# Performance work log

Hardware: AMD Instinct MI355X
Metric: run time of the kernel (lower is better)

The kernel has to match this reference:

```python
import jax, jax.numpy as jnp
import numpy as np

N_FFT = 512
HOP = 128
REF_MIC = 0
B, C, T = 8, 8, 64000


def hann(n):
    # periodic Hann, like torch.hann_window
    return 0.5 - 0.5 * jnp.cos(2.0 * jnp.pi * jnp.arange(n) / n)


def stft(x, n_fft, hop, window):
    # torch.stft with center=True, reflect padding, onesided
    pad = n_fft // 2
    pads = [(0, 0)] * (x.ndim - 1) + [(pad, pad)]
    xp = jnp.pad(x, pads, mode="reflect")
    n_frames = 1 + (xp.shape[-1] - n_fft) // hop
    idx = jnp.arange(n_frames)[:, None] * hop + jnp.arange(n_fft)[None, :]
    frames = xp[..., idx] * window                  # (..., N, n_fft)
    X = jnp.fft.rfft(frames, axis=-1)               # (..., N, F)
    return jnp.swapaxes(X, -1, -2)                  # (..., F, N)


def istft(X, n_fft, hop, window):
    # torch.istft: windowed overlap-add with squared-window normalization
    pad = n_fft // 2
    Xt = jnp.swapaxes(X, -1, -2)                    # (..., N, F)
    frames = jnp.fft.irfft(Xt, n=n_fft, axis=-1) * window  # (..., N, n_fft)
    n_frames = frames.shape[-2]
    out_len = n_fft + hop * (n_frames - 1)
    idx = jnp.arange(n_frames)[:, None] * hop + jnp.arange(n_fft)[None, :]
    y = jnp.zeros(frames.shape[:-2] + (out_len,), frames.dtype).at[..., idx].add(frames)
    wsum = jnp.zeros((out_len,), frames.dtype).at[idx].add(
        jnp.broadcast_to(window ** 2, (n_frames, n_fft)))
    y = y / jnp.maximum(wsum, 1e-10)
    return y[..., pad:out_len - pad]                # undo center padding


def mwf_forward(x, w1, b1, w2, b2):
    window = hann(N_FFT).astype(x.dtype)
    X = stft(x, N_FFT, HOP, window)                 # (B, C, F, N) complex
    X = X[..., 1:, :]                               # drop DC bin -> F' = n_fft//2
    b, c, fp, n = X.shape
    # --- mask model: 2-layer MLP on |X_ref| over frequency, per frame ---
    Xref = X[..., REF_MIC, :, :]                    # (B, F', N)
    feat = jnp.abs(Xref).swapaxes(-1, -2)           # (B, N, F')
    h = jax.nn.relu(feat @ w1 + b1)                 # (B, N, H)
    m = jax.nn.sigmoid(h @ w2 + b2)                 # (B, N, 2*F')
    masks = m.reshape(b, n, 2, fp).transpose(0, 2, 3, 1)[:, None]  # (B,1,2,F',N)
    mask_t = masks[..., 0, :, :]                    # (B, 1, F', N)
    mask_n = masks[..., 1, :, :]
    # --- masked spatial covariance matrices ---
    R_tgt = jnp.einsum("bsfn,bcfn,bdfn->bsfcd", mask_t, X, X.conj())
    R_noise = jnp.einsum("bsfn,bcfn,bdfn->bsfcd", mask_n, X, X.conj())
    # --- MWF beamforming weights: (R_t + R_n)^{-1} R_t e_ref ---
    rhs = R_tgt[..., REF_MIC]                       # (B, 1, F', C)
    bf = jnp.linalg.solve(R_tgt + R_noise, rhs[..., None])[..., 0]
    Xe = jnp.einsum("bcfn,bsfc->bsfn", X, bf.conj())  # (B, 1, F', N)
    # pad DC bin back with zeros
    Xe = jnp.concatenate([jnp.zeros(Xe.shape[:-2] + (1, n), Xe.dtype), Xe], axis=-2)
    y = istft(Xe, N_FFT, HOP, window)               # (B, 1, T')
    t = x.shape[-1]
    if y.shape[-1] < t:
        y = jnp.concatenate(
            [y, jnp.zeros(y.shape[:-1] + (t - y.shape[-1],), y.dtype)], axis=-1)
    else:
        y = y[..., :t]
    return y


def setup_inputs() -> dict:
    key = jax.random.key(0)
    k1, k2, k3 = jax.random.split(key, 3)
    fp, hid = N_FFT // 2, 512
    x = jax.random.normal(k1, (B, C, T), dtype=jnp.float32)
    w1 = jax.random.normal(k2, (fp, hid), dtype=jnp.float32) * (1.0 / np.sqrt(fp))
    b1 = jnp.zeros((hid,), dtype=jnp.float32)
    w2 = jax.random.normal(k3, (hid, 2 * fp), dtype=jnp.float32) * (1.0 / np.sqrt(hid))
    b2 = jnp.zeros((2 * fp,), dtype=jnp.float32)
    return {"x": x, "w1": w1, "b1": b1, "w2": w2, "b2": b2}


def reference(x, w1, b1, w2, b2):
    return mwf_forward(x, w1, b1, w2, b2)
```

## Files before the change

### kernel.cpp

```cpp
#include <hip/hip_runtime.h>
#include <hip/hip_bf16.h>
#include <math.h>

#define NFFT 512
#define HOP  128
#define PADW 256
#define TLEN 64000
#define NF   501
#define NFP  504
#define FP   256
#define CH   8
#define BATCH 8
#define HID  512
#define MROWS (BATCH * NF)
#define FPB  8
#define NGRP 63
#define CNCK 8
#define CCK  63
#define NSTG 4

#define S2C 0.70710678118654752f

typedef short bf16x8 __attribute__((ext_vector_type(8)));
typedef float f32x4 __attribute__((ext_vector_type(4)));

__device__ __forceinline__ unsigned short f2bf(float v) {
    __hip_bfloat16 hb = __float2bfloat16(v);
    return *reinterpret_cast<unsigned short*>(&hb);
}

__device__ __forceinline__ float2 cadd(float2 a, float2 b) { return make_float2(a.x + b.x, a.y + b.y); }
__device__ __forceinline__ float2 csub(float2 a, float2 b) { return make_float2(a.x - b.x, a.y - b.y); }
__device__ __forceinline__ float2 cmul(float2 a, float2 b) { return make_float2(a.x * b.x - a.y * b.y, a.x * b.y + a.y * b.x); }
__device__ __forceinline__ float2 mulnegi(float2 a) { return make_float2(a.y, -a.x); }

__device__ __forceinline__ void dft8(const float2 u[8], float2 v[8]) {
    float2 a0 = cadd(u[0], u[4]), a1 = cadd(u[1], u[5]), a2 = cadd(u[2], u[6]), a3 = cadd(u[3], u[7]);
    float2 b0 = csub(u[0], u[4]), b1 = csub(u[1], u[5]), b2 = csub(u[2], u[6]), b3 = csub(u[3], u[7]);
    float2 c0 = cadd(a0, a2), c1 = csub(a0, a2), c2 = cadd(a1, a3), c3 = csub(a1, a3);
    v[0] = cadd(c0, c2); v[4] = csub(c0, c2);
    float2 nic3 = mulnegi(c3);
    v[2] = cadd(c1, nic3); v[6] = csub(c1, nic3);
    float2 d1 = make_float2(S2C * (b1.x + b1.y), S2C * (b1.y - b1.x));
    float2 d2 = mulnegi(b2);
    float2 d3 = make_float2(S2C * (b3.y - b3.x), -S2C * (b3.x + b3.y));
    float2 e0 = cadd(b0, d2), e1 = csub(b0, d2), e2 = cadd(d1, d3), e3 = csub(d1, d3);
    v[1] = cadd(e0, e2); v[5] = csub(e0, e2);
    float2 nie3 = mulnegi(e3);
    v[3] = cadd(e1, nie3); v[7] = csub(e1, nie3);
}

__device__ __forceinline__ int refl(int j) {
    j = (j < 0) ? -j : j;
    j = (j >= TLEN) ? 2 * (TLEN - 1) - j : j;
    return j;
}

__global__ void k_tables(float* tw) {
    int j = threadIdx.x + blockIdx.x * blockDim.x;
    if (j < 512) {
        float ang = (float)(2.0 * M_PI * (double)j / 512.0);
        tw[j] = 0.5f - 0.5f * cosf(ang);
    }
}

__global__ __launch_bounds__(256) void k_wt(const float* __restrict__ w,
                                            unsigned short* __restrict__ wt, int K) {
    __shared__ float tile[32][33];
    int nt = blockIdx.x & 15;
    int kt = blockIdx.x >> 4;
    int tx = threadIdx.x & 31, ty = threadIdx.x >> 5;
    #pragma unroll
    for (int r = 0; r < 4; ++r)
        tile[ty + 8 * r][tx] = w[(size_t)(kt * 32 + ty + 8 * r) * HID + nt * 32 + tx];
    __syncthreads();
    #pragma unroll
    for (int r = 0; r < 4; ++r)
        wt[(size_t)(nt * 32 + ty + 8 * r) * K + kt * 32 + tx] = f2bf(tile[tx][ty + 8 * r]);
}

#define A_S 580
#define B_S 544
__global__ __launch_bounds__(256, 4) void k_stft(const float* __restrict__ x,
                                                 const float* __restrict__ tw,
                                                 float2* __restrict__ X,
                                                 unsigned short* __restrict__ featbf) {
    __shared__ float2 Abuf[4 * A_S];
    __shared__ float2 Bbuf[4 * B_S];
    __shared__ float2 Twd[512];
    int blk = blockIdx.x;
    int g = blk % NGRP;
    int bc = blk / NGRP;
    int c = bc % CH, b = bc / CH;
    int m0 = g * FPB;
    int tid = threadIdx.x;
    const float* xp = x + (size_t)(b * CH + c) * TLEN;

    #pragma unroll
    for (int r = 0; r < 2; ++r) {
        int e = tid + 256 * r;
        float se, ce;
        sincosf((float)e * (float)(2.0 * M_PI / 512.0), &se, &ce);
        Twd[e] = make_float2(ce, -se);
    }

    #pragma unroll
    for (int r = 0; r < 8; ++r) {
        int flat = r * 256 + tid;
        int sig = flat >> 9, t = flat & 511;
        int posa = (m0 + 2 * sig) * HOP + t - PADW;
        float xa = xp[refl(posa)];
        float xb = xp[refl(posa + HOP)];
        float w = tw[t];
        Abuf[sig * A_S + t] = make_float2(xa * w, xb * w);
    }
    __syncthreads();

    int sig = tid >> 6, dft = tid & 63;
    float2 u[8], v[8];

    {
        const float2* Az = &Abuf[sig * A_S];
        float2* Bu = &Bbuf[sig * B_S];
        #pragma unroll
        for (int a = 0; a < 8; ++a) u[a] = Az[64 * a + dft];
        dft8(u, v);
        #pragma unroll
        for (int k0 = 0; k0 < 8; ++k0) Bu[k0 * 68 + dft] = v[k0];
    }
    __syncthreads();

    {
        int k0 = dft >> 3, cd = dft & 7;
        const float2* Bu = &Bbuf[sig * B_S];
        float2* Au = &Abuf[sig * A_S];
        #pragma unroll
        for (int bb = 0; bb < 8; ++bb) u[bb] = Bu[k0 * 68 + 8 * bb + cd];
        #pragma unroll
        for (int bb = 1; bb < 8; ++bb) u[bb] = cmul(u[bb], Twd[(8 * bb * k0) & 511]);
        dft8(u, v);
        #pragma unroll
        for (int k1 = 0; k1 < 8; ++k1) Au[(8 * k0 + k1) * 9 + cd] = v[k1];
    }
    __syncthreads();

    {
        int k0 = dft >> 3, k1 = dft & 7;
        int kk = k0 + 8 * k1;
        const float2* Au = &Abuf[sig * A_S];
        float2* Bz = &Bbuf[sig * B_S];
        #pragma unroll
        for (int cd = 0; cd < 8; ++cd) u[cd] = Au[dft * 9 + cd];
        #pragma unroll
        for (int cd = 1; cd < 8; ++cd) u[cd] = cmul(u[cd], Twd[(cd * kk) & 511]);
        dft8(u, v);
        #pragma unroll
        for (int k2 = 0; k2 < 8; ++k2) Bz[kk + 64 * k2] = v[k2];
    }
    __syncthreads();

    {
        int kp = tid;
        int k = kp + 1;
        #pragma unroll
        for (int s = 0; s < 4; ++s) {
            float2 z1 = Bbuf[s * B_S + k];
            float2 z2 = Bbuf[s * B_S + (512 - k)];
            float Ar = 0.5f * (z1.x + z2.x);
            float Ai = 0.5f * (z1.y - z2.y);
            float Br = 0.5f * (z1.y + z2.y);
            float Bi = 0.5f * (z2.x - z1.x);
            int ma = m0 + 2 * s, mb_ = ma + 1;
            if (ma < NF) {
                X[((size_t)(b * NF + ma) * CH + c) * FP + kp] = make_float2(Ar, Ai);
                if (c == 0) featbf[((size_t)b * NF + ma) * FP + kp] = f2bf(sqrtf(Ar * Ar + Ai * Ai));
            }
            if (mb_ < NF) {
                X[((size_t)(b * NF + mb_) * CH + c) * FP + kp] = make_float2(Br, Bi);
                if (c == 0) featbf[((size_t)b * NF + mb_) * FP + kp] = f2bf(sqrtf(Br * Br + Bi * Bi));
            }
        }
    }
}

template<int K, int ACT>
__global__ __launch_bounds__(256) void k_mfma_mlp(const unsigned short* __restrict__ Abf,
                                                  const unsigned short* __restrict__ Wt,
                                                  const float* __restrict__ bias,
                                                  float* __restrict__ outf,
                                                  unsigned short* __restrict__ outbf,
                                                  int M) {
    __shared__ unsigned short Al[64][40];
    __shared__ unsigned short Bl[128][40];
    int bid = blockIdx.x;
    int nt = bid & 3, mt = bid >> 2;
    int m0 = mt * 64, n0 = nt * 128;
    int tid = threadIdx.x;
    int wid = tid >> 6, lane = tid & 63;
    int wm = wid >> 1, wn = wid & 1;
    int lr = lane & 15, lk = (lane >> 4) * 8;

    f32x4 acc[2][4] = {};

    int arow = tid >> 2, ak = (tid & 3) * 8;
    for (int k0 = 0; k0 < K; k0 += 32) {
        int garow = m0 + arow; if (garow > M - 1) garow = M - 1;
        float4 av = *(const float4*)&Abf[(size_t)garow * K + k0 + ak];
        int s0 = tid, s1 = tid + 256;
        float4 bv0 = *(const float4*)&Wt[(size_t)(n0 + (s0 >> 2)) * K + k0 + (s0 & 3) * 8];
        float4 bv1 = *(const float4*)&Wt[(size_t)(n0 + (s1 >> 2)) * K + k0 + (s1 & 3) * 8];
        if (k0 > 0) __syncthreads();
        *(float4*)&Al[arow][ak] = av;
        *(float4*)&Bl[s0 >> 2][(s0 & 3) * 8] = bv0;
        *(float4*)&Bl[s1 >> 2][(s1 & 3) * 8] = bv1;
        __syncthreads();
        bf16x8 af[2], bfr[4];
        af[0] = *(const bf16x8*)&Al[wm * 32 + lr][lk];
        af[1] = *(const bf16x8*)&Al[wm * 32 + 16 + lr][lk];
        #pragma unroll
        for (int nf = 0; nf < 4; ++nf)
            bfr[nf] = *(const bf16x8*)&Bl[wn * 64 + nf * 16 + lr][lk];
        #pragma unroll
        for (int mf = 0; mf < 2; ++mf)
            #pragma unroll
            for (int nf = 0; nf < 4; ++nf)
                acc[mf][nf] = __builtin_amdgcn_mfma_f32_16x16x32_bf16(af[mf], bfr[nf], acc[mf][nf], 0, 0, 0);
    }

    int rbase = (lane >> 4) * 4;
    #pragma unroll
    for (int mf = 0; mf < 2; ++mf) {
        #pragma unroll
        for (int nf = 0; nf < 4; ++nf) {
            int n = n0 + wn * 64 + nf * 16 + lr;
            float bj = bias[n];
            #pragma unroll
            for (int r = 0; r < 4; ++r) {
                int m = m0 + wm * 32 + mf * 16 + rbase + r;
                if (m < M) {
                    float vv = acc[mf][nf][r] + bj;
                    if (ACT == 0) {
                        outbf[(size_t)m * HID + n] = f2bf(fmaxf(vv, 0.f));
                    } else {
                        outf[(size_t)m * HID + n] = 1.f / (1.f + expf(-vv));
                    }
                }
            }
        }
    }
}

__global__ __launch_bounds__(512) void k_cov(const float2* __restrict__ X,
                                             const float* __restrict__ mo,
                                             float2* __restrict__ part) {
    int blk = blockIdx.x;
    int nc = blk & 7;
    int ftile = (blk >> 3) & 3;
    int b = blk >> 5;
    int tid = threadIdx.x;
    int c = tid >> 6;
    int ft = tid & 63;
    int f = ftile * 64 + ft;
    int n0 = nc * CCK;
    int n1 = n0 + CCK; if (n1 > NF) n1 = NF;

    __shared__ float2 vbuf[2][NSTG][CH][64];

    float ar[8], ai[8];
    #pragma unroll
    for (int d = 0; d < 8; ++d) { ar[d] = 0.f; ai[d] = 0.f; }
    float rr = 0.f, ri = 0.f;

    const float2* Xb = X + (size_t)b * NF * CH * FP;
    const float* mb = mo + (size_t)b * NF * HID;

    #pragma unroll
    for (int r = 0; r < NSTG; ++r) {
        int n = n0 + r;
        if (n < n1) vbuf[0][r][c][ft] = Xb[(size_t)(n * CH + c) * FP + f];
    }
    __syncthreads();
    int cur = 0;
    for (int nb = n0; nb < n1; nb += NSTG) {
        int nbn = nb + NSTG;
        float2 nx[NSTG];
        #pragma unroll
        for (int r = 0; r < NSTG; ++r) {
            int n = nbn + r;
            if (n < n1) nx[r] = Xb[(size_t)(n * CH + c) * FP + f];
        }
        float mts[NSTG], mns[NSTG];
        #pragma unroll
        for (int r = 0; r < NSTG; ++r) {
            int n = nb + r;
            if (n < n1) {
                mts[r] = mb[(size_t)n * HID + f];
                mns[r] = mb[(size_t)n * HID + FP + f];
            }
        }
        #pragma unroll
        for (int r = 0; r < NSTG; ++r) {
            int n = nb + r;
            if (n < n1) {
                float mt = mts[r], mn = mns[r];
                float w = mt + mn;
                float2 xc = vbuf[cur][r][c][ft];
                #pragma unroll
                for (int d = 0; d < 8; ++d) {
                    float2 xd = vbuf[cur][r][d][ft];
                    float pr = xc.x * xd.x + xc.y * xd.y;
                    float pi = xc.y * xd.x - xc.x * xd.y;
                    ar[d] += w * pr; ai[d] += w * pi;
                    if (d == 0) { rr += mt * pr; ri += mt * pi; }
                }
            }
        }
        if (nbn < n1) {
            #pragma unroll
            for (int r = 0; r < NSTG; ++r) {
                int n = nbn + r;
                if (n < n1) vbuf[cur ^ 1][r][c][ft] = nx[r];
            }
        }
        __syncthreads();
        cur ^= 1;
    }
    float2* pp = part + (((size_t)nc * BATCH + b) * FP + f) * 72;
    #pragma unroll
    for (int d = 0; d < 8; ++d)
        pp[c * 8 + d] = make_float2(ar[d], ai[d]);
    pp[64 + c] = make_float2(rr, ri);
}

__global__ __launch_bounds__(512) void k_cov_solve2(const float2* __restrict__ part,
                                                    float2* __restrict__ wc) {
    int blk = blockIdx.x;
    int fg = blk & 31;
    int b = blk >> 5;
    int tid = threadIdx.x;
    int c = tid >> 6, d = (tid >> 3) & 7, fl = tid & 7;
    int f = fg * 8 + fl;
    float ar = 0.f, ai = 0.f, rr = 0.f, ri = 0.f;
    const float2* pb = part + ((size_t)b * FP + f) * 72;
    #pragma unroll
    for (int nc = 0; nc < CNCK; ++nc) {
        const float2* p = pb + (size_t)nc * BATCH * FP * 72;
        float2 v = p[c * 8 + d];
        ar += v.x; ai += v.y;
        if (d == 0) { float2 u = p[64 + c]; rr += u.x; ri += u.y; }
    }
    __shared__ float2 Am[8][73];
    __shared__ float2 rh[8][8];
    __shared__ float2 sl[8][9];
    Am[fl][c * 9 + d] = make_float2(ar, ai);
    if (d == 0) rh[fl][c] = make_float2(rr, ri);
    __syncthreads();
    if (tid < 8) {
        int ln = tid;
        float2* A = Am[ln];
        float2* r = rh[ln];
        float2* sol = sl[ln];
        for (int kk = 0; kk < 8; ++kk) {
            float2 pp = A[kk * 9 + kk];
            float ip = 1.f / (pp.x * pp.x + pp.y * pp.y);
            float invr = pp.x * ip, invi = -pp.y * ip;
            for (int i = kk + 1; i < 8; ++i) {
                float2 aik = A[i * 9 + kk];
                float fr2 = aik.x * invr - aik.y * invi;
                float fi2 = aik.x * invi + aik.y * invr;
                for (int jj = kk; jj < 8; ++jj) {
                    float2 ak = A[kk * 9 + jj];
                    A[i * 9 + jj].x -= fr2 * ak.x - fi2 * ak.y;
                    A[i * 9 + jj].y -= fr2 * ak.y + fi2 * ak.x;
                }
                r[i].x -= fr2 * r[kk].x - fi2 * r[kk].y;
                r[i].y -= fr2 * r[kk].y + fi2 * r[kk].x;
            }
        }
        for (int kk = 7; kk >= 0; --kk) {
            float sr = r[kk].x, si = r[kk].y;
            for (int jj = kk + 1; jj < 8; ++jj) {
                float2 ak = A[kk * 9 + jj];
                float2 xj = sol[jj];
                sr -= ak.x * xj.x - ak.y * xj.y;
                si -= ak.x * xj.y + ak.y * xj.x;
            }
            float2 pp = A[kk * 9 + kk];
            float ip = 1.f / (pp.x * pp.x + pp.y * pp.y);
            sol[kk].x = (sr * pp.x + si * pp.y) * ip;
            sol[kk].y = (si * pp.x - sr * pp.y) * ip;
        }
        for (int cc = 0; cc < 8; ++cc)
            wc[((size_t)b * CH + cc) * FP + fg * 8 + ln] = make_float2(sol[cc].x, -sol[cc].y);
    }
}

__global__ __launch_bounds__(512) void k_istft_bf(const float2* __restrict__ X,
                                                  const float2* __restrict__ wc,
                                                  float* __restrict__ yfr) {
    __shared__ float2 Zp[4 * 512];
    __shared__ float2 Gl[16 * 32 * 5];
    int blk = blockIdx.x;
    int g = blk % NGRP, b = blk / NGRP;
    int m0 = g * FPB;
    int tid = threadIdx.x;

    if (tid < 4) Zp[tid * 512] = make_float2(0.f, 0.f);
    const float2* Xb0 = X + (size_t)b * NF * CH * FP;
    const float2* wcb = wc + (size_t)b * CH * FP;
    #pragma unroll
    for (int half = 0; half < 2; ++half) {
        int i = half * 512 + tid;
        int sig = i >> 8, kp = i & 255;
        int ma = m0 + 2 * sig, mb_ = ma + 1;
        float2 Xa = make_float2(0.f, 0.f), Xb = make_float2(0.f, 0.f);
        if (ma < NF) {
            #pragma unroll
            for (int c = 0; c < 8; ++c) {
                float2 xv = Xb0[(size_t)(ma * CH + c) * FP + kp];
                float2 wv = wcb[c * FP + kp];
                Xa.x += xv.x * wv.x - xv.y * wv.y;
                Xa.y += xv.x * wv.y + xv.y * wv.x;
            }
        }
        if (mb_ < NF) {
            #pragma unroll
            for (int c = 0; c < 8; ++c) {
                float2 xv = Xb0[(size_t)(mb_ * CH + c) * FP + kp];
                float2 wv = wcb[c * FP + kp];
                Xb.x += xv.x * wv.x - xv.y * wv.y;
                Xb.y += xv.x * wv.y + xv.y * wv.x;
            }
        }
        int k = kp + 1;
        if (k == 256) {
            Zp[sig * 512 + 256] = make_float2(Xa.x, Xb.x);
        } else {
            Zp[sig * 512 + k]       = make_float2(Xa.x - Xb.y, Xa.y + Xb.x);
            Zp[sig * 512 + 512 - k] = make_float2(Xa.x + Xb.y, Xb.x - Xa.y);
        }
    }
    __syncthreads();

    {
        int k1 = tid >> 5, tau = tid & 31;
        float sa, ca;
        sincosf((float)tau * (float)(2.0 * M_PI / 32.0), &sa, &ca);
        float stepc = ca, steps = sa;
        float gr[4], gi[4];
        #pragma unroll
        for (int s = 0; s < 4; ++s) { gr[s] = 0.f; gi[s] = 0.f; }
        float cr = 1.f, ci = 0.f;
        #pragma unroll 4
        for (int k2 = 0; k2 < 32; ++k2) {
            int k = k1 + 16 * k2;
            #pragma unroll
            for (int s = 0; s < 4; ++s) {
                float2 z = Zp[s * 512 + k];
                gr[s] += z.x * cr - z.y * ci;
                gi[s] += z.x * ci + z.y * cr;
            }
            float ncr = cr * stepc - ci * steps;
            ci = cr * steps + ci * stepc;
            cr = ncr;
        }
        #pragma unroll
        for (int s = 0; s < 4; ++s)
            Gl[(k1 * 32 + tau) * 5 + s] = make_float2(gr[s], gi[s]);
    }
    __syncthreads();

    int t = tid;
    int tau = t & 31;
    float sa2, ca2;
    sincosf((float)t * (float)(2.0 * M_PI / 512.0), &sa2, &ca2);
    float stepc = ca2, steps = sa2;
    float accr[4], acci[4];
    #pragma unroll
    for (int s = 0; s < 4; ++s) { accr[s] = 0.f; acci[s] = 0.f; }
    float cr = 1.f, ci = 0.f;
    #pragma unroll 4
    for (int k1 = 0; k1 < 16; ++k1) {
        #pragma unroll
        for (int s = 0; s < 4; ++s) {
            float2 gv = Gl[(k1 * 32 + tau) * 5 + s];
            accr[s] += gv.x * cr - gv.y * ci;
            acci[s] += gv.x * ci + gv.y * cr;
        }
        float ncr = cr * stepc - ci * steps;
        ci = cr * steps + ci * stepc;
        cr = ncr;
    }
    float wv = (0.5f - 0.5f * ca2) * (1.f / 512.f);
    #pragma unroll
    for (int s = 0; s < 4; ++s) {
        int ma = m0 + 2 * s, mb_ = ma + 1;
        if (ma < NF)  yfr[((size_t)b * NFP + ma) * 512 + t] = accr[s] * wv;
        if (mb_ < NF) yfr[((size_t)b * NFP + mb_) * 512 + t] = acci[s] * wv;
    }
}

__global__ __launch_bounds__(256) void k_out(const float* __restrict__ yfr,
                                             float* __restrict__ out) {
    int i = blockIdx.x * blockDim.x + threadIdx.x;
    if (i >= BATCH * TLEN) return;
    int b = i / TLEN;
    int t = i - b * TLEN;
    int p = t + PADW;
    int q = p & 127;
    int m0 = p >> 7;
    float sq, cq;
    sincosf((float)q * (float)(2.0 * M_PI / 512.0), &sq, &cq);
    float w4[4] = {0.5f - 0.5f * cq, 0.5f + 0.5f * sq, 0.5f + 0.5f * cq, 0.5f - 0.5f * sq};
    float val = 0.f, wsum = 0.f;
    const float* yb = yfr + (size_t)b * NFP * 512;
    #pragma unroll
    for (int dm = 0; dm < 4; ++dm) {
        int mm = m0 - dm;
        if (mm >= 0 && mm < NF) {
            val += yb[(size_t)mm * 512 + q + 128 * dm];
            wsum += w4[dm] * w4[dm];
        }
    }
    out[i] = val / fmaxf(wsum, 1e-10f);
}

extern "C" void kernel_launch(void* const* d_in, const int* in_sizes, int n_in,
                              void* d_out, int out_size, void* d_ws, size_t ws_size,
                              hipStream_t stream) {
    const float* x  = (const float*)d_in[0];
    const float* w1 = (const float*)d_in[1];
    const float* b1 = (const float*)d_in[2];
    const float* w2 = (const float*)d_in[3];
    const float* b2 = (const float*)d_in[4];

    float* ws = (float*)d_ws;
    size_t off = 0;
    float*  tw    = ws + off; off += 512;
    float2* X     = (float2*)(ws + off); off += (size_t)BATCH * FP * NF * CH * 2;
    float*  mo    = ws + off; off += (size_t)BATCH * NF * HID;
    float2* wc    = (float2*)(ws + off); off += (size_t)BATCH * FP * CH * 2;
    float*  yfr   = ws + off; off += (size_t)BATCH * NFP * 512;
    float2* part  = (float2*)(ws + off); off += (size_t)CNCK * BATCH * FP * 72 * 2;
    unsigned short* featbf = (unsigned short*)(ws + off); off += (size_t)MROWS * FP / 2;
    unsigned short* hbf    = (unsigned short*)(ws + off); off += (size_t)MROWS * HID / 2;
    unsigned short* wt1bf  = (unsigned short*)(ws + off); off += (size_t)HID * FP / 2;
    unsigned short* wt2bf  = (unsigned short*)(ws + off); off += (size_t)HID * HID / 2;

    k_tables<<<2, 256, 0, stream>>>(tw);
    k_wt<<<16 * 8, 256, 0, stream>>>(w1, wt1bf, FP);
    k_wt<<<16 * 16, 256, 0, stream>>>(w2, wt2bf, HID);
    k_stft<<<BATCH * CH * NGRP, 256, 0, stream>>>(x, tw, X, featbf);
    k_mfma_mlp<FP, 0><<<63 * 4, 256, 0, stream>>>(featbf, wt1bf, b1, mo, hbf, MROWS);
    k_mfma_mlp<HID, 1><<<63 * 4, 256, 0, stream>>>(hbf, wt2bf, b2, mo, hbf, MROWS);
    k_cov<<<BATCH * 4 * CNCK, 512, 0, stream>>>(X, mo, part);
    k_cov_solve2<<<BATCH * 32, 512, 0, stream>>>(part, wc);
    k_istft_bf<<<BATCH * NGRP, 512, 0, stream>>>(X, wc, yfr);
    k_out<<<(BATCH * TLEN + 255) / 256, 256, 0, stream>>>(yfr, (float*)d_out);
}
```

Baseline: 129.5 us.

## Merge prep kernels, stage STFT input in LDS, split covariance over more chunks

Combines the window-table and two weight-transpose kernels into one launch, removing two launch boundaries. The STFT kernel now loads its contiguous input span once into shared memory instead of issuing two strided global reads per frame sample. The covariance reduction splits frames into 16 chunks instead of 8 when workspace allows, doubling block count for better occupancy at the cost of a larger partial buffer and more reduction work in the solve kernel.

```diff
diff --git a/kernel.cpp b/kernel.cpp
--- a/kernel.cpp
+++ b/kernel.cpp
@@ -15,8 +15,6 @@
 #define MROWS (BATCH * NF)
 #define FPB  8
 #define NGRP 63
-#define CNCK 8
-#define CCK  63
 #define NSTG 4
 
 #define S2C 0.70710678118654752f
@@ -56,19 +54,26 @@
     return j;
 }
 
-__global__ void k_tables(float* tw) {
-    int j = threadIdx.x + blockIdx.x * blockDim.x;
-    if (j < 512) {
-        float ang = (float)(2.0 * M_PI * (double)j / 512.0);
-        tw[j] = 0.5f - 0.5f * cosf(ang);
-    }
-}
-
-__global__ __launch_bounds__(256) void k_wt(const float* __restrict__ w,
-                                            unsigned short* __restrict__ wt, int K) {
+__global__ __launch_bounds__(256) void k_prep(const float* __restrict__ w1,
+                                              const float* __restrict__ w2,
+                                              float* __restrict__ tw,
+                                              unsigned short* __restrict__ wt1,
+                                              unsigned short* __restrict__ wt2) {
     __shared__ float tile[32][33];
-    int nt = blockIdx.x & 15;
-    int kt = blockIdx.x >> 4;
+    int bid = blockIdx.x;
+    if (bid == 384) {
+        #pragma unroll
+        for (int r = 0; r < 2; ++r) {
+            int e = threadIdx.x + 256 * r;
+            float ang = (float)(2.0 * M_PI * (double)e / 512.0);
+            tw[e] = 0.5f - 0.5f * cosf(ang);
+        }
+        return;
+    }
+    const float* w; unsigned short* wt; int K, lb;
+    if (bid < 128) { w = w1; wt = wt1; K = 256; lb = bid; }
+    else           { w = w2; wt = wt2; K = 512; lb = bid - 128; }
+    int nt = lb & 15, kt = lb >> 4;
     int tx = threadIdx.x & 31, ty = threadIdx.x >> 5;
     #pragma unroll
     for (int r = 0; r < 4; ++r)
@@ -104,15 +109,22 @@
         Twd[e] = make_float2(ce, -se);
     }
 
+    float* xs = (float*)Bbuf;
+    int base = m0 * HOP - PADW;
+    #pragma unroll
+    for (int r = 0; r < 6; ++r) {
+        int i = r * 256 + tid;
+        xs[i] = xp[refl(base + i)];
+    }
+    __syncthreads();
+
     #pragma unroll
     for (int r = 0; r < 8; ++r) {
         int flat = r * 256 + tid;
         int sig = flat >> 9, t = flat & 511;
-        int posa = (m0 + 2 * sig) * HOP + t - PADW;
-        float xa = xp[refl(posa)];
-        float xb = xp[refl(posa + HOP)];
         float w = tw[t];
-        Abuf[sig * A_S + t] = make_float2(xa * w, xb * w);
+        Abuf[sig * A_S + t] = make_float2(xs[2 * sig * 128 + t] * w,
+                                          xs[(2 * sig + 1) * 128 + t] * w);
     }
     __syncthreads();
 
@@ -252,17 +264,14 @@
 
 __global__ __launch_bounds__(512) void k_cov(const float2* __restrict__ X,
                                              const float* __restrict__ mo,
-                                             float2* __restrict__ part) {
-    int blk = blockIdx.x;
-    int nc = blk & 7;
-    int ftile = (blk >> 3) & 3;
-    int b = blk >> 5;
+                                             float2* __restrict__ part, int cck) {
+    int nc = blockIdx.x, ftile = blockIdx.y, b = blockIdx.z;
     int tid = threadIdx.x;
     int c = tid >> 6;
     int ft = tid & 63;
     int f = ftile * 64 + ft;
-    int n0 = nc * CCK;
-    int n1 = n0 + CCK; if (n1 > NF) n1 = NF;
+    int n0 = nc * cck;
+    int n1 = n0 + cck; if (n1 > NF) n1 = NF;
 
     __shared__ float2 vbuf[2][NSTG][CH][64];
 
@@ -333,7 +342,7 @@
 }
 
 __global__ __launch_bounds__(512) void k_cov_solve2(const float2* __restrict__ part,
-                                                    float2* __restrict__ wc) {
+                                                    float2* __restrict__ wc, int ncnt) {
     int blk = blockIdx.x;
     int fg = blk & 31;
     int b = blk >> 5;
@@ -342,8 +351,7 @@
     int f = fg * 8 + fl;
     float ar = 0.f, ai = 0.f, rr = 0.f, ri = 0.f;
     const float2* pb = part + ((size_t)b * FP + f) * 72;
-    #pragma unroll
-    for (int nc = 0; nc < CNCK; ++nc) {
+    for (int nc = 0; nc < ncnt; ++nc) {
         const float2* p = pb + (size_t)nc * BATCH * FP * 72;
         float2 v = p[c * 8 + d];
         ar += v.x; ai += v.y;
@@ -541,20 +549,22 @@
     float*  mo    = ws + off; off += (size_t)BATCH * NF * HID;
     float2* wc    = (float2*)(ws + off); off += (size_t)BATCH * FP * CH * 2;
     float*  yfr   = ws + off; off += (size_t)BATCH * NFP * 512;
-    float2* part  = (float2*)(ws + off); off += (size_t)CNCK * BATCH * FP * 72 * 2;
     unsigned short* featbf = (unsigned short*)(ws + off); off += (size_t)MROWS * FP / 2;
     unsigned short* hbf    = (unsigned short*)(ws + off); off += (size_t)MROWS * HID / 2;
     unsigned short* wt1bf  = (unsigned short*)(ws + off); off += (size_t)HID * FP / 2;
     unsigned short* wt2bf  = (unsigned short*)(ws + off); off += (size_t)HID * HID / 2;
-
-    k_tables<<<2, 256, 0, stream>>>(tw);
-    k_wt<<<16 * 8, 256, 0, stream>>>(w1, wt1bf, FP);
-    k_wt<<<16 * 16, 256, 0, stream>>>(w2, wt2bf, HID);
+    float2* part  = (float2*)(ws + off);
+
+    int cnck = 8, cck = 63;
+    size_t need16 = (off + (size_t)16 * BATCH * FP * 72 * 2) * sizeof(float);
+    if (ws_size >= need16) { cnck = 16; cck = 32; }
+
+    k_prep<<<385, 256, 0, stream>>>(w1, w2, tw, wt1bf, wt2bf);
     k_stft<<<BATCH * CH * NGRP, 256, 0, stream>>>(x, tw, X, featbf);
     k_mfma_mlp<FP, 0><<<63 * 4, 256, 0, stream>>>(featbf, wt1bf, b1, mo, hbf, MROWS);
     k_mfma_mlp<HID, 1><<<63 * 4, 256, 0, stream>>>(hbf, wt2bf, b2, mo, hbf, MROWS);
-    k_cov<<<BATCH * 4 * CNCK, 512, 0, stream>>>(X, mo, part);
-    k_cov_solve2<<<BATCH * 32, 512, 0, stream>>>(part, wc);
+    k_cov<<<dim3(cnck, 4, BATCH), 512, 0, stream>>>(X, mo, part, cck);
+    k_cov_solve2<<<BATCH * 32, 512, 0, stream>>>(part, wc, cnck);
     k_istft_bf<<<BATCH * NGRP, 512, 0, stream>>>(X, wc, yfr);
     k_out<<<(BATCH * TLEN + 255) / 256, 256, 0, stream>>>(yfr, (float*)d_out);
 }
```

Result: faster. 123.7 us (-4.5%).
